# Kernel tuning notes

Measured on AMD Instinct MI355X. Metric: run time of the kernel, lower is better.

Reference implementation:

```python
import jax, jax.numpy as jnp
import numpy as np

N, E, F, H, B = 100000, 600000, 128, 128, 250


def setup_inputs() -> dict:
    key = jax.random.key(0)
    ks = jax.random.split(key, 10)
    x = jax.random.normal(ks[0], (N, F), dtype=jnp.float32)
    # last two columns encode cluster id c in {0,1,2}: c = x[:,-1] + 2*x[:,-2]
    c = jax.random.randint(ks[1], (N,), 0, 3)
    x = x.at[:, -2].set((c == 2).astype(jnp.float32))
    x = x.at[:, -1].set((c == 1).astype(jnp.float32))
    edge_index = jax.random.randint(ks[2], (2, E), 0, N, dtype=jnp.int64)
    batch = (jnp.arange(N, dtype=jnp.int64) // (N // B))  # 400 nodes per graph
    s = 1.0 / np.sqrt(F)
    sh = 1.0 / np.sqrt(H)
    W1 = jax.random.uniform(ks[3], (F, H), jnp.float32, -s, s)
    b1 = jnp.zeros((H,), jnp.float32)
    W2 = jax.random.uniform(ks[4], (H, H), jnp.float32, -sh, sh)
    b2 = jnp.zeros((H,), jnp.float32)
    W3 = jax.random.uniform(ks[5], (H, H), jnp.float32, -sh, sh)
    b3 = jnp.zeros((H,), jnp.float32)
    sl = 1.0 / np.sqrt(3 * H)
    Wl = jax.random.uniform(ks[6], (3 * H, 1), jnp.float32, -sl, sl)
    bl = jax.random.uniform(ks[7], (1,), jnp.float32, -sl, sl)
    return {"x": x, "edge_index": edge_index, "batch": batch,
            "W1": W1, "b1": b1, "W2": W2, "b2": b2, "W3": W3, "b3": b3,
            "Wl": Wl, "bl": bl}


def _gcn_conv(h, W, b, src, dst, dinv):
    # PyG GCNConv: h @ W, then D^{-1/2} (A + I) D^{-1/2} aggregation, + bias.
    h = h @ W
    norm = dinv[src] * dinv[dst]              # [E+N]
    msg = h[src] * norm[:, None]              # gather + scale
    out = jax.ops.segment_sum(msg, dst, num_segments=N)  # scatter-add at target
    return out + b


def _forward(x, edge_index, batch, W1, b1, W2, b2, W3, b3, Wl, bl):
    cluster = (x[:, -1] + 2.0 * x[:, -2]).astype(jnp.int64)  # in {0,1,2}
    loop = jnp.arange(N, dtype=edge_index.dtype)
    src = jnp.concatenate([edge_index[0], loop])  # self-loops appended
    dst = jnp.concatenate([edge_index[1], loop])
    deg = jax.ops.segment_sum(jnp.ones_like(dst, dtype=x.dtype), dst, num_segments=N)
    dinv = jax.lax.rsqrt(jnp.maximum(deg, 1.0))  # deg >= 1 via self-loops

    h = jax.nn.relu(_gcn_conv(x, W1, b1, src, dst, dinv))
    h = jax.nn.relu(_gcn_conv(h, W2, b2, src, dst, dinv))
    h = _gcn_conv(h, W3, b3, src, dst, dinv)

    cb = batch * 3 + cluster                   # segment id per (graph, cluster)
    sums = jax.ops.segment_sum(h, cb, num_segments=B * 3)
    cnts = jax.ops.segment_sum(jnp.ones((N,), h.dtype), cb, num_segments=B * 3)
    xc = sums / jnp.maximum(cnts, 1.0)[:, None]  # scatter-mean
    z = xc.reshape(B, 3 * H)                   # dropout p=0.2 is identity in eval
    return jax.nn.sigmoid(z @ Wl + bl)


def reference(x, edge_index, batch, W1, b1, W2, b2, W3, b3, Wl, bl):
    return _forward(x, edge_index, batch, W1, b1, W2, b2, W3, b3, Wl, bl)
```

## Files before the change

### kernel.cpp

```cpp
#include <hip/hip_runtime.h>
#include <hip/hip_bf16.h>
#include <math.h>


#define WAVE 64
#define NPARTS 25
#define WPAD 136

typedef __attribute__((ext_vector_type(8))) short bf16x8;
typedef __attribute__((ext_vector_type(4))) float f32x4;

__device__ __forceinline__ float bflo(unsigned u) { return __uint_as_float(u << 16); }
__device__ __forceinline__ float bfhi(unsigned u) { return __uint_as_float(u & 0xffff0000u); }
__device__ __forceinline__ float bfs(unsigned short s) {
    return __uint_as_float(((unsigned)s) << 16);
}
__device__ __forceinline__ unsigned short bf16r(float f) {
    unsigned u = __float_as_uint(f);
    return (unsigned short)((u + 0x7fffu + ((u >> 16) & 1u)) >> 16);
}
__device__ __forceinline__ unsigned pack_bf16(float a, float b) {
    return (unsigned)bf16r(a) | ((unsigned)bf16r(b) << 16);
}
__device__ __forceinline__ void fma8(float* acc, float w, uint4 u) {
    acc[0] += w * bflo(u.x); acc[1] += w * bfhi(u.x);
    acc[2] += w * bflo(u.y); acc[3] += w * bfhi(u.y);
    acc[4] += w * bflo(u.z); acc[5] += w * bfhi(u.z);
    acc[6] += w * bflo(u.w); acc[7] += w * bfhi(u.w);
}

__device__ __forceinline__ void agg_node(const uint4* __restrict__ hb4,
                                         const int* __restrict__ row_ptr,
                                         const int* __restrict__ cnt,
                                         const int2* __restrict__ ce,
                                         const float* __restrict__ dinv,
                                         int nc, bool ok, int sl, float* acc) {
    float di = dinv[nc];
    uint4 self = hb4[(size_t)nc * 16 + sl];
    float w0 = di * di;
    acc[0] = w0 * bflo(self.x); acc[1] = w0 * bfhi(self.x);
    acc[2] = w0 * bflo(self.y); acc[3] = w0 * bfhi(self.y);
    acc[4] = w0 * bflo(self.z); acc[5] = w0 * bfhi(self.z);
    acc[6] = w0 * bflo(self.w); acc[7] = w0 * bfhi(self.w);
    int s0 = row_ptr[nc];
    int deg = ok ? cnt[nc] : 0;
    int2 c0, c1, c2, c3;
    if (deg > 0) {
        int dm = deg - 1;
        c0 = ce[s0];
        c1 = ce[s0 + min(1, dm)];
        c2 = ce[s0 + min(2, dm)];
        c3 = ce[s0 + min(3, dm)];
    }
    for (int i = 0; i < deg; i += 4) {
        int2 p0 = c0, p1 = c1, p2 = c2, p3 = c3;
        int nx = i + 4;
        if (nx < deg) {
            int dm = deg - 1;
            c0 = ce[s0 + nx];
            c1 = ce[s0 + min(nx + 1, dm)];
            c2 = ce[s0 + min(nx + 2, dm)];
            c3 = ce[s0 + min(nx + 3, dm)];
        }
        uint4 u0 = hb4[(size_t)p0.x * 16 + sl];
        uint4 u1 = hb4[(size_t)p1.x * 16 + sl];
        uint4 u2 = hb4[(size_t)p2.x * 16 + sl];
        uint4 u3 = hb4[(size_t)p3.x * 16 + sl];
        float w1 = (i + 1 < deg) ? __int_as_float(p1.y) : 0.f;
        float w2 = (i + 2 < deg) ? __int_as_float(p2.y) : 0.f;
        float w3 = (i + 3 < deg) ? __int_as_float(p3.y) : 0.f;
        fma8(acc, __int_as_float(p0.y), u0);
        fma8(acc, w1, u1);
        fma8(acc, w2, u2);
        fma8(acc, w3, u3);
    }
}


__global__ void countprep(const int* __restrict__ dst, int* __restrict__ cnt, int ne,
                          const float* __restrict__ W1, const float* __restrict__ W2,
                          const float* __restrict__ W3, const float* __restrict__ Wl,
                          unsigned short* __restrict__ Wt, float* __restrict__ wv,
                          const float* __restrict__ x, unsigned* __restrict__ hb,
                          int* __restrict__ cluster, int n32, int cb) {
    int b = blockIdx.x;
    if (b < cb) {
        int e = b * 256 + threadIdx.x;
        if (e < ne) atomicAdd(&cnt[dst[e]], 1);
    } else if (b < cb + 128) {
        int bb = b - cb;
        int idx = (bb & 63) * 256 + threadIdx.x;
        int layer = bb >> 6;
        const float* W = (layer == 0) ? W1 : W2;
        int n = idx >> 7, k = idx & 127;
        Wt[layer * 16384 + n * 128 + k] = bf16r(W[k * 128 + n]);
    } else if (b < cb + 130) {
        int idx = (b - cb - 128) * 256 + threadIdx.x;
        if (idx < 384) {
            int c = idx >> 7, k = idx & 127;
            const float* wlc = Wl + c * 128;
            const float* w3r = W3 + k * 128;
            float s = 0.f;
#pragma unroll 8
            for (int n = 0; n < 128; ++n) s += w3r[n] * wlc[n];
            wv[c * 128 + k] = s;
        }
    } else {
        int i = (b - cb - 130) * 256 + threadIdx.x;
        if (i < n32) {
            float4 v = ((const float4*)x)[i];
            hb[i * 2 + 0] = pack_bf16(v.x, v.y);
            hb[i * 2 + 1] = pack_bf16(v.z, v.w);
            if ((i & 31) == 31)
                cluster[i >> 5] = (int)(v.w + 2.0f * v.z + 0.5f);
        }
    }
}

__global__ void scan_block(const int* __restrict__ in, int* __restrict__ out,
                           int* __restrict__ bsums, float* __restrict__ dinv, int n) {
    __shared__ int lds[256];
    int t = threadIdx.x;
    int base = blockIdx.x * 1024 + t * 4;
    int v0 = (base + 0 < n) ? in[base + 0] : 0;
    int v1 = (base + 1 < n) ? in[base + 1] : 0;
    int v2 = (base + 2 < n) ? in[base + 2] : 0;
    int v3 = (base + 3 < n) ? in[base + 3] : 0;
    int s = v0 + v1 + v2 + v3;
    lds[t] = s;
    __syncthreads();
    for (int off = 1; off < 256; off <<= 1) {
        int add = (t >= off) ? lds[t - off] : 0;
        __syncthreads();
        lds[t] += add;
        __syncthreads();
    }
    int excl = lds[t] - s;
    if (base + 0 < n) { out[base + 0] = excl;           dinv[base + 0] = rsqrtf((float)(v0 + 1)); }
    if (base + 1 < n) { out[base + 1] = excl + v0;      dinv[base + 1] = rsqrtf((float)(v1 + 1)); }
    if (base + 2 < n) { out[base + 2] = excl + v0 + v1; dinv[base + 2] = rsqrtf((float)(v2 + 1)); }
    if (base + 3 < n) { out[base + 3] = excl + v0 + v1 + v2;
                        dinv[base + 3] = rsqrtf((float)(v3 + 1)); }
    if (t == 255) bsums[blockIdx.x] = lds[255];
}

__global__ void scan_add2(int* __restrict__ out, const int* __restrict__ bsums, int n) {
    __shared__ int red[256];
    int t = threadIdx.x;
    red[t] = (t < blockIdx.x) ? bsums[t] : 0;
    __syncthreads();
    for (int off = 128; off > 0; off >>= 1) {
        if (t < off) red[t] += red[t + off];
        __syncthreads();
    }
    int add = red[0];
    int base = blockIdx.x * 1024 + t * 4;
#pragma unroll
    for (int i = 0; i < 4; ++i)
        if (base + i < n) out[base + i] += add;
}

__global__ void fill_kernel(const int* __restrict__ src, const int* __restrict__ dst,
                            const int* __restrict__ row_ptr, int* __restrict__ fill,
                            int2* __restrict__ ce, const float* __restrict__ dinv,
                            int ne) {
    int e = blockIdx.x * blockDim.x + threadIdx.x;
    if (e < ne) {
        int d = dst[e], s = src[e];
        int pos = row_ptr[d] + atomicAdd(&fill[d], 1);
        ce[pos] = make_int2(s, __float_as_int(dinv[s] * dinv[d]));
    }
}


__global__ void agg_kernel(const uint4* __restrict__ hb4, uint4* __restrict__ out4,
                           const int* __restrict__ row_ptr, const int* __restrict__ cnt,
                           const int2* __restrict__ ce, const float* __restrict__ dinv,
                           int n) {
    int wid = blockIdx.x * (blockDim.x >> 6) + (threadIdx.x >> 6);
    int lane = threadIdx.x & 63;
    int g = lane >> 4, sl = lane & 15;
    int node = wid * 4 + g;
    bool ok = node < n;
    int nc = ok ? node : (n - 1);
    float acc[8];
    agg_node(hb4, row_ptr, cnt, ce, dinv, nc, ok, sl, acc);
    if (ok) {
        uint4 o;
        o.x = pack_bf16(acc[0], acc[1]);
        o.y = pack_bf16(acc[2], acc[3]);
        o.z = pack_bf16(acc[4], acc[5]);
        o.w = pack_bf16(acc[6], acc[7]);
        out4[(size_t)node * 16 + sl] = o;
    }
}


__global__ __launch_bounds__(256) void agg_pool(
    const uint4* __restrict__ hb4,
    const int* __restrict__ row_ptr, const int* __restrict__ cnt,
    const int2* __restrict__ ce, const float* __restrict__ dinv,
    const int* __restrict__ cluster,
    float* __restrict__ psums, int* __restrict__ pcnts, int n) {
    __shared__ float smW[4][3][128];
    __shared__ int smC[4][3];
    const int t = threadIdx.x;
    for (int i = t; i < 4 * 3 * 128; i += 256) ((float*)smW)[i] = 0.f;
    if (t < 12) ((int*)smC)[t] = 0;
    __syncthreads();

    const int wave = t >> 6, lane = t & 63;
    const int g = lane >> 4, sl = lane & 15;
    const int node = blockIdx.x * 16 + wave * 4 + g;
    const bool ok = node < n;
    const int nc = ok ? node : (n - 1);
    float acc[8];
    agg_node(hb4, row_ptr, cnt, ce, dinv, nc, ok, sl, acc);

    const int cl = ok ? cluster[nc] : 0;
#pragma unroll
    for (int g2 = 0; g2 < 4; ++g2) {
        if (g == g2 && ok) {
            float* dstp = &smW[wave][cl][sl * 8];
#pragma unroll
            for (int j = 0; j < 8; ++j) dstp[j] += acc[j];
            if (sl == 0) smC[wave][cl] += 1;
        }
    }
    __syncthreads();

    if (t < 128) {
#pragma unroll
        for (int c = 0; c < 3; ++c) {
            float s = smW[0][c][t] + smW[1][c][t] + smW[2][c][t] + smW[3][c][t];
            psums[((size_t)blockIdx.x * 3 + c) * 128 + t] = s;
        }
    }
    if (t < 3)
        pcnts[blockIdx.x * 3 + t] = smC[0][t] + smC[1][t] + smC[2][t] + smC[3][t];
}


__global__ __launch_bounds__(256) void gemm_mfma(const unsigned short* __restrict__ A,
                                                 const unsigned short* __restrict__ Wt,
                                                 const float* __restrict__ bias,
                                                 unsigned short* __restrict__ Cb) {
    __shared__ unsigned short sm[128 * WPAD];
    const int t = threadIdx.x;
    const int wave = t >> 6, lane = t & 63;
    const int quad = lane >> 4, lr = lane & 15;
    const size_t row0 = (size_t)blockIdx.x * 128 + wave * 32;

    {
        int r = t >> 1, h = t & 1;
        const uint4* s = (const uint4*)(Wt + r * 128 + h * 64);
        uint4* d = (uint4*)(sm + r * WPAD + h * 64);
#pragma unroll
        for (int i = 0; i < 8; ++i) d[i] = s[i];
    }
    __syncthreads();

    f32x4 acc[2][8];
#pragma unroll
    for (int i2 = 0; i2 < 2; ++i2)
#pragma unroll
        for (int ct = 0; ct < 8; ++ct) acc[i2][ct] = (f32x4){0.f, 0.f, 0.f, 0.f};

    const unsigned short* arow0 = A + (row0 + lr) * 128;
    const unsigned short* arow1 = arow0 + 16 * 128;
#pragma unroll
    for (int kc = 0; kc < 4; ++kc) {
        int kb = kc * 32 + quad * 8;
        bf16x8 a0 = *(const bf16x8*)(arow0 + kb);
        bf16x8 a1 = *(const bf16x8*)(arow1 + kb);
#pragma unroll
        for (int ct = 0; ct < 8; ++ct) {
            bf16x8 w = *(const bf16x8*)(sm + (ct * 16 + lr) * WPAD + kb);
            acc[0][ct] = __builtin_amdgcn_mfma_f32_16x16x32_bf16(w, a0, acc[0][ct], 0, 0, 0);
            acc[1][ct] = __builtin_amdgcn_mfma_f32_16x16x32_bf16(w, a1, acc[1][ct], 0, 0, 0);
        }
    }

#pragma unroll
    for (int i2 = 0; i2 < 2; ++i2) {
        unsigned short* crow = Cb + (row0 + i2 * 16 + lr) * 128;
#pragma unroll
        for (int ct = 0; ct < 8; ++ct) {
            float4 bq = *(const float4*)&bias[ct * 16 + quad * 4];
            float v0 = fmaxf(acc[i2][ct][0] + bq.x, 0.f);
            float v1 = fmaxf(acc[i2][ct][1] + bq.y, 0.f);
            float v2 = fmaxf(acc[i2][ct][2] + bq.z, 0.f);
            float v3 = fmaxf(acc[i2][ct][3] + bq.w, 0.f);
            uint2 p;
            p.x = pack_bf16(v0, v1);
            p.y = pack_bf16(v2, v3);
            *(uint2*)(crow + ct * 16 + quad * 4) = p;
        }
    }
}

__global__ void head_kernel(const float* __restrict__ part_sums,
                            const int* __restrict__ part_cnts,
                            const float* __restrict__ wv, const float* __restrict__ b3,
                            const float* __restrict__ Wl, const float* __restrict__ bl,
                            float* __restrict__ out) {
    int b = blockIdx.x, t = threadIdx.x;
    float s0 = 0.f, s1 = 0.f, s2 = 0.f;
    int n0 = 0, n1 = 0, n2 = 0;
#pragma unroll
    for (int p = 0; p < NPARTS; ++p) {
        int blk = b * NPARTS + p;
        size_t o = (size_t)blk * 384 + t;
        s0 += part_sums[o];
        s1 += part_sums[o + 128];
        s2 += part_sums[o + 256];
        n0 += part_cnts[blk * 3 + 0];
        n1 += part_cnts[blk * 3 + 1];
        n2 += part_cnts[blk * 3 + 2];
    }
    float bt = b3[t];
    float z = 0.f;
    if (n0 > 0) z += (s0 / (float)n0) * wv[t]       + bt * Wl[t];
    if (n1 > 0) z += (s1 / (float)n1) * wv[128 + t] + bt * Wl[128 + t];
    if (n2 > 0) z += (s2 / (float)n2) * wv[256 + t] + bt * Wl[256 + t];
    for (int off = 32; off > 0; off >>= 1) z += __shfl_down(z, off);
    __shared__ float partial[2];
    if ((t & 63) == 0) partial[t >> 6] = z;
    __syncthreads();
    if (t == 0) {
        float zz = partial[0] + partial[1] + bl[0];
        out[b] = 1.0f / (1.0f + expf(-zz));
    }
}


extern "C" void kernel_launch(void* const* d_in, const int* in_sizes, int n_in,
                              void* d_out, int out_size, void* d_ws, size_t ws_size,
                              hipStream_t stream) {
    const float* x  = (const float*)d_in[0];
    const int*   ei = (const int*)d_in[1];
    const float* W1 = (const float*)d_in[3];
    const float* b1 = (const float*)d_in[4];
    const float* W2 = (const float*)d_in[5];
    const float* b2 = (const float*)d_in[6];
    const float* W3 = (const float*)d_in[7];
    const float* b3 = (const float*)d_in[8];
    const float* Wl = (const float*)d_in[9];
    const float* bl = (const float*)d_in[10];
    float* out = (float*)d_out;

    const int N = in_sizes[0] / 128;
    const int E = in_sizes[1] / 2;
    const int B = out_size;
    const int Npad = (N + 127) & ~127;
    const int npg = N / B;
    (void)npg;

    const int* srcp = ei;
    const int* dstp = ei + E;

    char* ws = (char*)d_ws;
    size_t off = 0;
    auto alloc = [&](size_t bytes) -> char* {
        char* p = ws + off;
        off += (bytes + 255) & ~(size_t)255;
        return p;
    };
    unsigned short* hb  = (unsigned short*)alloc((size_t)Npad * 128 * 2);
    unsigned short* ab  = (unsigned short*)alloc((size_t)Npad * 128 * 2);
    unsigned short* wt  = (unsigned short*)alloc((size_t)2 * 16384 * 2);
    float* wv      = (float*)alloc(384 * 4);
    float* dinv    = (float*)alloc((size_t)N * 4);
    int*   row_ptr = (int*)  alloc((size_t)N * 4);
    int*   cluster = (int*)  alloc((size_t)N * 4);
    int2*  ce      = (int2*) alloc((size_t)E * 8);
    int*   bsums   = (int*)  alloc(512 * 4);
    float* psums   = (float*)alloc((size_t)B * NPARTS * 3 * 128 * 4);
    int*   pcnts   = (int*)  alloc((size_t)B * NPARTS * 3 * 4);
    int*   cnt     = (int*)  alloc((size_t)N * 4);
    int*   fill    = (int*)  alloc((size_t)N * 4);
    size_t zspan = (size_t)((char*)fill + (size_t)N * 4 - (char*)cnt);
    (void)ws_size; (void)n_in;

    hipMemsetAsync(cnt, 0, zspan, stream);

    int cb = (E + 255) / 256;
    int prepBlocks = (N * 32 + 255) / 256;
    countprep<<<cb + 130 + prepBlocks, 256, 0, stream>>>(
        dstp, cnt, E, W1, W2, W3, Wl, wt, wv, x, (unsigned*)hb, cluster,
        N * 32, cb);

    int scanBlocks = (N + 1023) / 1024;
    scan_block<<<scanBlocks, 256, 0, stream>>>(cnt, row_ptr, bsums, dinv, N);
    scan_add2<<<scanBlocks, 256, 0, stream>>>(row_ptr, bsums, N);

    fill_kernel<<<(E + 255) / 256, 256, 0, stream>>>(srcp, dstp, row_ptr, fill,
                                                     ce, dinv, E);

    int gemmBlocks = Npad / 128;
    int aggBlocks = (N + 15) / 16;

    agg_kernel<<<aggBlocks, 256, 0, stream>>>((const uint4*)hb, (uint4*)ab,
                                              row_ptr, cnt, ce, dinv, N);
    gemm_mfma<<<gemmBlocks, 256, 0, stream>>>(ab, wt,         b1, hb);
    agg_kernel<<<aggBlocks, 256, 0, stream>>>((const uint4*)hb, (uint4*)ab,
                                              row_ptr, cnt, ce, dinv, N);
    gemm_mfma<<<gemmBlocks, 256, 0, stream>>>(ab, wt + 16384, b2, hb);

    agg_pool<<<aggBlocks, 256, 0, stream>>>((const uint4*)hb, row_ptr, cnt, ce,
                                            dinv, cluster, psums, pcnts, N);
    head_kernel<<<B, 128, 0, stream>>>(psums, pcnts, wv, b3, Wl, bl, out);
}
```

Before: 305.0 us.

## Widen aggregation unroll to 8, vectorize prep loads, interleave count blocks

The neighbor aggregation loop now prefetches and gathers eight edges per iteration instead of four, which raises memory-level parallelism for the irregular gathers. The fused prep kernel now processes four destination indices per thread with an int4 load, and converts eight floats per thread to bf16 with a single 16-byte store. Count blocks are interleaved with the conversion blocks, one in every twelve, so the atomics overlap with streaming work instead of all running first. The costs are higher register pressure in the aggregation loop and more complex block-role indexing.

Result: slower. 316.1 us (+3.6%).

```diff
diff --git a/kernel.cpp b/kernel.cpp
--- a/kernel.cpp
+++ b/kernel.cpp
@@ -44,35 +44,56 @@
     acc[6] = w0 * bflo(self.w); acc[7] = w0 * bfhi(self.w);
     int s0 = row_ptr[nc];
     int deg = ok ? cnt[nc] : 0;
-    int2 c0, c1, c2, c3;
+    int2 c0, c1, c2, c3, c4, c5, c6, c7;
     if (deg > 0) {
         int dm = deg - 1;
         c0 = ce[s0];
         c1 = ce[s0 + min(1, dm)];
         c2 = ce[s0 + min(2, dm)];
         c3 = ce[s0 + min(3, dm)];
-    }
-    for (int i = 0; i < deg; i += 4) {
+        c4 = ce[s0 + min(4, dm)];
+        c5 = ce[s0 + min(5, dm)];
+        c6 = ce[s0 + min(6, dm)];
+        c7 = ce[s0 + min(7, dm)];
+    }
+    for (int i = 0; i < deg; i += 8) {
         int2 p0 = c0, p1 = c1, p2 = c2, p3 = c3;
-        int nx = i + 4;
+        int2 p4 = c4, p5 = c5, p6 = c6, p7 = c7;
+        int nx = i + 8;
         if (nx < deg) {
             int dm = deg - 1;
             c0 = ce[s0 + nx];
             c1 = ce[s0 + min(nx + 1, dm)];
             c2 = ce[s0 + min(nx + 2, dm)];
             c3 = ce[s0 + min(nx + 3, dm)];
+            c4 = ce[s0 + min(nx + 4, dm)];
+            c5 = ce[s0 + min(nx + 5, dm)];
+            c6 = ce[s0 + min(nx + 6, dm)];
+            c7 = ce[s0 + min(nx + 7, dm)];
         }
         uint4 u0 = hb4[(size_t)p0.x * 16 + sl];
         uint4 u1 = hb4[(size_t)p1.x * 16 + sl];
         uint4 u2 = hb4[(size_t)p2.x * 16 + sl];
         uint4 u3 = hb4[(size_t)p3.x * 16 + sl];
+        uint4 u4 = hb4[(size_t)p4.x * 16 + sl];
+        uint4 u5 = hb4[(size_t)p5.x * 16 + sl];
+        uint4 u6 = hb4[(size_t)p6.x * 16 + sl];
+        uint4 u7 = hb4[(size_t)p7.x * 16 + sl];
         float w1 = (i + 1 < deg) ? __int_as_float(p1.y) : 0.f;
         float w2 = (i + 2 < deg) ? __int_as_float(p2.y) : 0.f;
         float w3 = (i + 3 < deg) ? __int_as_float(p3.y) : 0.f;
+        float w4 = (i + 4 < deg) ? __int_as_float(p4.y) : 0.f;
+        float w5 = (i + 5 < deg) ? __int_as_float(p5.y) : 0.f;
+        float w6 = (i + 6 < deg) ? __int_as_float(p6.y) : 0.f;
+        float w7 = (i + 7 < deg) ? __int_as_float(p7.y) : 0.f;
         fma8(acc, __int_as_float(p0.y), u0);
         fma8(acc, w1, u1);
         fma8(acc, w2, u2);
         fma8(acc, w3, u3);
+        fma8(acc, w4, u4);
+        fma8(acc, w5, u5);
+        fma8(acc, w6, u6);
+        fma8(acc, w7, u7);
     }
 }
 
@@ -82,20 +103,35 @@
                           const float* __restrict__ W3, const float* __restrict__ Wl,
                           unsigned short* __restrict__ Wt, float* __restrict__ wv,
                           const float* __restrict__ x, unsigned* __restrict__ hb,
-                          int* __restrict__ cluster, int n32, int cb) {
+                          int* __restrict__ cluster, int n8, int cntB) {
     int b = blockIdx.x;
-    if (b < cb) {
-        int e = b * 256 + threadIdx.x;
-        if (e < ne) atomicAdd(&cnt[dst[e]], 1);
-    } else if (b < cb + 128) {
-        int bb = b - cb;
-        int idx = (bb & 63) * 256 + threadIdx.x;
-        int layer = bb >> 6;
+    int t = threadIdx.x;
+    if ((b % 12) == 11) {
+        int c = b / 12;
+        if (c >= cntB) return;
+        int e4 = c * 256 + t;
+        int e = e4 * 4;
+        if (e + 3 < ne) {
+            int4 d4 = ((const int4*)dst)[e4];
+            atomicAdd(&cnt[d4.x], 1);
+            atomicAdd(&cnt[d4.y], 1);
+            atomicAdd(&cnt[d4.z], 1);
+            atomicAdd(&cnt[d4.w], 1);
+        } else {
+            for (int k = 0; k < 4; ++k)
+                if (e + k < ne) atomicAdd(&cnt[dst[e + k]], 1);
+        }
+        return;
+    }
+    int p = b - (b + 1) / 12;
+    if (p < 128) {
+        int idx = (p & 63) * 256 + t;
+        int layer = p >> 6;
         const float* W = (layer == 0) ? W1 : W2;
         int n = idx >> 7, k = idx & 127;
         Wt[layer * 16384 + n * 128 + k] = bf16r(W[k * 128 + n]);
-    } else if (b < cb + 130) {
-        int idx = (b - cb - 128) * 256 + threadIdx.x;
+    } else if (p < 130) {
+        int idx = (p - 128) * 256 + t;
         if (idx < 384) {
             int c = idx >> 7, k = idx & 127;
             const float* wlc = Wl + c * 128;
@@ -106,13 +142,19 @@
             wv[c * 128 + k] = s;
         }
     } else {
-        int i = (b - cb - 130) * 256 + threadIdx.x;
-        if (i < n32) {
-            float4 v = ((const float4*)x)[i];
-            hb[i * 2 + 0] = pack_bf16(v.x, v.y);
-            hb[i * 2 + 1] = pack_bf16(v.z, v.w);
-            if ((i & 31) == 31)
-                cluster[i >> 5] = (int)(v.w + 2.0f * v.z + 0.5f);
+        int i8 = (p - 130) * 256 + t;
+        if (i8 < n8) {
+            const float4* x4 = (const float4*)x;
+            float4 v0 = x4[i8 * 2 + 0];
+            float4 v1 = x4[i8 * 2 + 1];
+            uint4 o;
+            o.x = pack_bf16(v0.x, v0.y);
+            o.y = pack_bf16(v0.z, v0.w);
+            o.z = pack_bf16(v1.x, v1.y);
+            o.w = pack_bf16(v1.z, v1.w);
+            ((uint4*)hb)[i8] = o;
+            if ((i8 & 15) == 15)
+                cluster[i8 >> 4] = (int)(v1.w + 2.0f * v1.z + 0.5f);
         }
     }
 }
@@ -353,8 +395,6 @@
     const int E = in_sizes[1] / 2;
     const int B = out_size;
     const int Npad = (N + 127) & ~127;
-    const int npg = N / B;
-    (void)npg;
 
     const int* srcp = ei;
     const int* dstp = ei + E;
@@ -384,11 +424,14 @@
 
     hipMemsetAsync(cnt, 0, zspan, stream);
 
-    int cb = (E + 255) / 256;
-    int prepBlocks = (N * 32 + 255) / 256;
-    countprep<<<cb + 130 + prepBlocks, 256, 0, stream>>>(
-        dstp, cnt, E, W1, W2, W3, Wl, wt, wv, x, (unsigned*)hb, cluster,
-        N * 32, cb);
+    const int n8 = N * 16;
+    const int prepBlocks = (n8 + 255) / 256;
+    const int cntB = ((E + 3) / 4 + 255) / 256;
+    const int roleP = 130 + prepBlocks;
+    int total = cntB * 12;
+    while (total - total / 12 < roleP) total += 12;
+    countprep<<<total, 256, 0, stream>>>(dstp, cnt, E, W1, W2, W3, Wl, wt, wv,
+                                         x, (unsigned*)hb, cluster, n8, cntB);
 
     int scanBlocks = (N + 1023) / 1024;
     scan_block<<<scanBlocks, 256, 0, stream>>>(cnt, row_ptr, bsums, dinv, N);
```
